# Kernel tuning notes

Measured on AMD Instinct MI355X. Metric: run time of the kernel, lower is better.

The kernel has to match this reference:

```python
import jax, jax.numpy as jnp
import numpy as np


def _cell(xt, h, c, Wih, Whh, b):
    # Single LSTM cell step; PyTorch gate order i, f, g, o.
    g = xt @ Wih.T + h @ Whh.T + b
    i, f, gg, o = jnp.split(g, 4, axis=-1)
    c = jax.nn.sigmoid(f) * c + jax.nn.sigmoid(i) * jnp.tanh(gg)
    h = jax.nn.sigmoid(o) * jnp.tanh(c)
    return h, c


def _lstm_layer(x, Wih, Whh, b):
    # x: [B, T, D] -> hs: [B, T, H], (h, c): final states [B, H]
    B = x.shape[0]
    H = Whh.shape[1]
    h0 = jnp.zeros((B, H), x.dtype)
    c0 = jnp.zeros((B, H), x.dtype)

    def step(carry, xt):
        h, c = carry
        h, c = _cell(xt, h, c, Wih, Whh, b)
        return (h, c), h

    (h, c), hs = jax.lax.scan(step, (h0, c0), jnp.swapaxes(x, 0, 1))
    return jnp.swapaxes(hs, 0, 1), h, c


def setup_inputs() -> dict:
    key = jax.random.key(0)
    B, T_SRC, D_IN, H, TGT = 512, 256, 32, 128, 64
    ks = iter(jax.random.split(key, 32))
    s_in = 1.0 / np.sqrt(H)

    def u(k, shape):
        return jax.random.uniform(k, shape, jnp.float32, -s_in, s_in)

    inp = {"x": jax.random.normal(next(ks), (B, T_SRC, D_IN), jnp.float32),
           "target_len": TGT}
    for pre in ("enc", "dec"):
        for l, din in ((0, D_IN), (1, H)):
            inp[f"{pre}_Wih{l}"] = u(next(ks), (4 * H, din))
            inp[f"{pre}_Whh{l}"] = u(next(ks), (4 * H, H))
            inp[f"{pre}_bih{l}"] = u(next(ks), (4 * H,))
            inp[f"{pre}_bhh{l}"] = u(next(ks), (4 * H,))
    inp["lin_W"] = u(next(ks), (D_IN, H))
    inp["lin_b"] = u(next(ks), (D_IN,))
    return inp


def reference(x, target_len,
              enc_Wih0, enc_Whh0, enc_bih0, enc_bhh0,
              enc_Wih1, enc_Whh1, enc_bih1, enc_bhh1,
              dec_Wih0, dec_Whh0, dec_bih0, dec_bhh0,
              dec_Wih1, dec_Whh1, dec_bih1, dec_bhh1,
              lin_W, lin_b):
    # --- encoder: 2-layer full-sequence LSTM, zero initial state ---
    hs0, eh0, ec0 = _lstm_layer(x, enc_Wih0, enc_Whh0, enc_bih0 + enc_bhh0)
    _, eh1, ec1 = _lstm_layer(hs0, enc_Wih1, enc_Whh1, enc_bih1 + enc_bhh1)

    # --- decoder: recursive single-step LSTM + linear head, fed back ---
    db0 = dec_bih0 + dec_bhh0
    db1 = dec_bih1 + dec_bhh1
    dec_in0 = x[:, -1, :]  # last source step

    def step(carry, _):
        h0, c0, h1, c1, inp = carry
        h0, c0 = _cell(inp, h0, c0, dec_Wih0, dec_Whh0, db0)
        h1, c1 = _cell(h0, h1, c1, dec_Wih1, dec_Whh1, db1)
        out = h1 @ lin_W.T + lin_b
        return (h0, c0, h1, c1, out), out

    _, outs = jax.lax.scan(step, (eh0, ec0, eh1, ec1, dec_in0), None,
                           length=target_len)
    return jnp.swapaxes(outs, 0, 1)  # [B, target_len, input_size]
```

## Files before the change

### kernel.cpp

```cpp
#include <hip/hip_runtime.h>
#include <cstdint>
#include <cstddef>

typedef short  short8  __attribute__((ext_vector_type(8)));
typedef float  float4v __attribute__((ext_vector_type(4)));

#define MFMA_B16(a,b,c) __builtin_amdgcn_mfma_f32_16x16x32_bf16(a,b,c,0,0,0)

static constexpr int B_  = 512;
static constexpr int T_  = 256;
static constexpr int DIN = 32;
static constexpr int H_  = 128;
static constexpr int TGT = 64;

static constexpr size_t OFF_XFRAG = 0;
static constexpr size_t OFF_EW0   = 8388608;
static constexpr size_t OFF_EW1LO = OFF_EW0   + 163840;
static constexpr size_t OFF_EW1HI = OFF_EW1LO + 131072;
static constexpr size_t OFF_DW0   = OFF_EW1HI + 131072;
static constexpr size_t OFF_DW1LO = OFF_DW0   + 163840;
static constexpr size_t OFF_DW1HI = OFF_DW1LO + 131072;
static constexpr size_t OFF_LIN   = OFF_DW1HI + 131072;
static constexpr size_t OFF_BIAS  = OFF_LIN   + 8192;
static constexpr size_t WS_NEED   = OFF_BIAS  + 8320;

static constexpr int SM_W    = 0;
static constexpr int SM_ABUF = 131072;
static constexpr int SM_INP  = 147712;
static constexpr int SM_LIN  = 148992;
static constexpr int SM_TOTAL= 157184;

__device__ __forceinline__ short f2bf(float f){
  unsigned u = __float_as_uint(f);
  unsigned r = (u + 0x7fffu + ((u>>16)&1u)) >> 16;
  return (short)(r & 0xffffu);
}
__device__ __forceinline__ float fast_sigm(float x){
  float e = __expf(-x);
  return __builtin_amdgcn_rcpf(1.f + e);
}
__device__ __forceinline__ float fast_tanh(float x){
  float e = __expf(-2.f*x);
  return __builtin_amdgcn_rcpf(1.f + e)*2.f - 1.f;
}

__global__ void prep_x_kernel(const float* __restrict__ x, short8* __restrict__ xfrag){
  int i = blockIdx.x*256 + threadIdx.x;
  if (i >= 32*256*64) return;
  int l    = i & 63;
  int t    = (i >> 6) & 255;
  int bblk = i >> 14;
  int b    = bblk*16 + (l & 15);
  const float* src = x + ((size_t)(b*T_ + t))*DIN + ((l>>4)*8);
  short8 v;
  #pragma unroll
  for (int j=0;j<8;j++) v[j] = f2bf(src[j]);
  xfrag[i] = v;
}

__device__ __forceinline__ void pack160(short8* __restrict__ dst,
                                        const float* __restrict__ Wih,
                                        const float* __restrict__ Whh,
                                        int e){
  int nt = e/320; int r = e%320; int kb = r/64; int l = r%64;
  int n  = nt*16 + (l&15);
  short8 v;
  #pragma unroll
  for (int j=0;j<8;j++){
    int k = kb*32 + (l>>4)*8 + j;
    float f = (k < 32) ? Wih[n*32 + k] : Whh[n*128 + (k-32)];
    v[j] = f2bf(f);
  }
  dst[e] = v;
}
__device__ __forceinline__ void pack256s(short8* __restrict__ dlo, short8* __restrict__ dhi,
                                         const float* __restrict__ Wih,
                                         const float* __restrict__ Whh,
                                         int e){
  int nt = e/512; int r = e%512; int kb = r/64; int l = r%64;
  int n  = nt*16 + (l&15);
  short8 v;
  #pragma unroll
  for (int j=0;j<8;j++){
    int k = kb*32 + (l>>4)*8 + j;
    float f = (k < 128) ? Wih[n*128 + k] : Whh[n*128 + (k-128)];
    v[j] = f2bf(f);
  }
  if (kb < 4) dlo[(nt*4 + kb)*64 + l]     = v;
  else        dhi[(nt*4 + (kb-4))*64 + l] = v;
}

__global__ void prep_w_kernel(
    const float* __restrict__ eWih0, const float* __restrict__ eWhh0,
    const float* __restrict__ eWih1, const float* __restrict__ eWhh1,
    const float* __restrict__ dWih0, const float* __restrict__ dWhh0,
    const float* __restrict__ dWih1, const float* __restrict__ dWhh1,
    const float* __restrict__ linW,
    const float* __restrict__ eb0a, const float* __restrict__ eb0b,
    const float* __restrict__ eb1a, const float* __restrict__ eb1b,
    const float* __restrict__ db0a, const float* __restrict__ db0b,
    const float* __restrict__ db1a, const float* __restrict__ db1b,
    const float* __restrict__ linb,
    short8* __restrict__ encW0,
    short8* __restrict__ encW1lo, short8* __restrict__ encW1hi,
    short8* __restrict__ decW0,
    short8* __restrict__ decW1lo, short8* __restrict__ decW1hi,
    short8* __restrict__ linT,  float* __restrict__ biases)
{
  int i = blockIdx.x*256 + threadIdx.x;
  if (i < 10240)       { pack160(encW0, eWih0, eWhh0, i); }
  else if (i < 26624)  { pack256s(encW1lo, encW1hi, eWih1, eWhh1, i-10240); }
  else if (i < 36864)  { pack160(decW0, dWih0, dWhh0, i-26624); }
  else if (i < 53248)  { pack256s(decW1lo, decW1hi, dWih1, dWhh1, i-36864); }
  else if (i < 53760)  {
    int e = i - 53248;
    int nt = e/256; int r = e%256; int kb = r/64; int l = r%64;
    int n = nt*16 + (l&15);
    short8 v;
    #pragma unroll
    for (int j=0;j<8;j++){
      int k = kb*32 + (l>>4)*8 + j;
      v[j] = f2bf(linW[n*128 + k]);
    }
    linT[e] = v;
  }
  else if (i < 55840)  {
    int e = i - 53760;
    float v;
    if      (e < 512)  v = eb0a[e]       + eb0b[e];
    else if (e < 1024) v = eb1a[e-512]   + eb1b[e-512];
    else if (e < 1536) v = db0a[e-1024]  + db0b[e-1024];
    else if (e < 2048) v = db1a[e-1536]  + db1b[e-1536];
    else               v = linb[e-2048];
    biases[e] = v;
  }
}

__global__ __launch_bounds__(512, 1) void lstm_main_kernel(
    const short8* __restrict__ xfrag,
    const short8* __restrict__ encW0,
    const short8* __restrict__ encW1lo, const short8* __restrict__ encW1hi,
    const short8* __restrict__ decW0,
    const short8* __restrict__ decW1lo, const short8* __restrict__ decW1hi,
    const short8* __restrict__ linT,  const float* __restrict__ biases,
    float* __restrict__ out)
{
  extern __shared__ __align__(16) char smem[];
  short8* Wlds        = (short8*)(smem + SM_W);
  short (*Abuf)[520]  = (short(*)[520])(smem + SM_ABUF);
  short (*inpA)[40]   = (short(*)[40])(smem + SM_INP);
  short8* Wlin        = (short8*)(smem + SM_LIN);

  const int tid  = threadIdx.x;
  const int w    = tid >> 6;
  const int l    = tid & 63;
  const int col  = l & 15;
  const int lq   = l >> 4;
  const int bblk = blockIdx.x;

  for (int i = tid; i < 8192; i += 512) Wlds[i] = encW1hi[i];
  for (int i = tid; i < 16*520; i += 512) ((short*)Abuf)[i] = 0;

  short8 W0r[4][5];
  short8 W1lo[4][4];
  #pragma unroll
  for (int i=0;i<4;i++){
    #pragma unroll
    for (int kb=0;kb<5;kb++) W0r[i][kb]  = encW0  [(size_t)(8*i+w)*320 + (size_t)kb*64 + l];
    #pragma unroll
    for (int kb=0;kb<4;kb++) W1lo[i][kb] = encW1lo[(size_t)(8*i+w)*256 + (size_t)kb*64 + l];
  }
  float bs0[4], bs1[4];
  #pragma unroll
  for (int i=0;i<4;i++){
    bs0[i] = biases[       (8*i+w)*16 + col];
    bs1[i] = biases[512 +  (8*i+w)*16 + col];
  }

  float c0[4] = {0.f,0.f,0.f,0.f};
  float c1[4] = {0.f,0.f,0.f,0.f};

  const short8* xf = xfrag + (size_t)bblk*T_*64 + l;
  short8 a0 = xf[0];
  __syncthreads();


  {
    short8 hp[4];
    #pragma unroll
    for (int kb=0;kb<4;kb++) hp[kb] = *(const short8*)&Abuf[col][128 + kb*32 + lq*8];
    float4v acc0[4];
    #pragma unroll
    for (int i4=0;i4<4;i4++){
      float4v a = {bs0[i4],bs0[i4],bs0[i4],bs0[i4]};
      a = MFMA_B16(a0, W0r[i4][0], a);
      #pragma unroll
      for (int kb=0;kb<4;kb++) a = MFMA_B16(hp[kb], W0r[i4][kb+1], a);
      acc0[i4] = a;
    }
    a0 = xf[64];
    #pragma unroll
    for (int q=0;q<4;q++){
      float cc = fast_sigm(acc0[1][q])*c0[q] + fast_sigm(acc0[0][q])*fast_tanh(acc0[2][q]);
      c0[q] = cc;
      Abuf[lq*4+q][0 + 16*w + col] = f2bf(fast_sigm(acc0[3][q])*fast_tanh(cc));
    }
    __syncthreads();
  }

  #pragma unroll 2
  for (int i = 1; i < T_; i++){
    const int p_h0_r = ((i-1)&1)*128;
    const int p_h0_w = (i&1)*128;
    const int p_h1_r = 256 + (i&1)*128;
    const int p_h1_w = 256 + ((i-1)&1)*128;

    short8 hp[4], h1p[4];
    #pragma unroll
    for (int kb=0;kb<4;kb++) hp[kb]  = *(const short8*)&Abuf[col][p_h0_r + kb*32 + lq*8];
    #pragma unroll
    for (int kb=0;kb<4;kb++) h1p[kb] = *(const short8*)&Abuf[col][p_h1_r + kb*32 + lq*8];

    float4v acc0[4], acc1[4];
    #pragma unroll
    for (int i4=0;i4<4;i4++){
      float4v a = {bs0[i4],bs0[i4],bs0[i4],bs0[i4]};
      a = MFMA_B16(a0, W0r[i4][0], a);
      #pragma unroll
      for (int kb=0;kb<4;kb++) a = MFMA_B16(hp[kb], W0r[i4][kb+1], a);
      acc0[i4] = a;

      float4v b = {bs1[i4],bs1[i4],bs1[i4],bs1[i4]};
      #pragma unroll
      for (int kb=0;kb<4;kb++) b = MFMA_B16(hp[kb], W1lo[i4][kb], b);
      #pragma unroll
      for (int kb=0;kb<4;kb++){
        short8 wv = Wlds[((8*i4+w)*4 + kb)*64 + l];
        b = MFMA_B16(h1p[kb], wv, b);
      }
      acc1[i4] = b;
    }
    a0 = xf[(size_t)((i+1 < T_) ? i+1 : i)*64];

    #pragma unroll
    for (int q=0;q<4;q++){
      float cc = fast_sigm(acc0[1][q])*c0[q] + fast_sigm(acc0[0][q])*fast_tanh(acc0[2][q]);
      c0[q] = cc;
      Abuf[lq*4+q][p_h0_w + 16*w + col] = f2bf(fast_sigm(acc0[3][q])*fast_tanh(cc));
    }
    #pragma unroll
    for (int q=0;q<4;q++){
      float cc = fast_sigm(acc1[1][q])*c1[q] + fast_sigm(acc1[0][q])*fast_tanh(acc1[2][q]);
      c1[q] = cc;
      Abuf[lq*4+q][p_h1_w + 16*w + col] = f2bf(fast_sigm(acc1[3][q])*fast_tanh(cc));
    }
    __syncthreads();
  }

  {
    const int p_h0_r = 128;
    const int p_h1_r = 256 + 0;
    const int p_h1_w = 256 + 128;
    short8 hp[4], h1p[4];
    #pragma unroll
    for (int kb=0;kb<4;kb++) hp[kb]  = *(const short8*)&Abuf[col][p_h0_r + kb*32 + lq*8];
    #pragma unroll
    for (int kb=0;kb<4;kb++) h1p[kb] = *(const short8*)&Abuf[col][p_h1_r + kb*32 + lq*8];
    float4v acc1[4];
    #pragma unroll
    for (int i4=0;i4<4;i4++){
      float4v b = {bs1[i4],bs1[i4],bs1[i4],bs1[i4]};
      #pragma unroll
      for (int kb=0;kb<4;kb++) b = MFMA_B16(hp[kb], W1lo[i4][kb], b);
      #pragma unroll
      for (int kb=0;kb<4;kb++){
        short8 wv = Wlds[((8*i4+w)*4 + kb)*64 + l];
        b = MFMA_B16(h1p[kb], wv, b);
      }
      acc1[i4] = b;
    }
    #pragma unroll
    for (int q=0;q<4;q++){
      float cc = fast_sigm(acc1[1][q])*c1[q] + fast_sigm(acc1[0][q])*fast_tanh(acc1[2][q]);
      c1[q] = cc;
      Abuf[lq*4+q][p_h1_w + 16*w + col] = f2bf(fast_sigm(acc1[3][q])*fast_tanh(cc));
    }
    __syncthreads();
  }

  for (int i = tid; i < 8192; i += 512) Wlds[i] = decW1hi[i];
  if (tid < 512) Wlin[tid] = linT[tid];
  #pragma unroll
  for (int i=0;i<4;i++){
    #pragma unroll
    for (int kb=0;kb<5;kb++) W0r[i][kb]  = decW0  [(size_t)(8*i+w)*320 + (size_t)kb*64 + l];
    #pragma unroll
    for (int kb=0;kb<4;kb++) W1lo[i][kb] = decW1lo[(size_t)(8*i+w)*256 + (size_t)kb*64 + l];
    bs0[i] = biases[1024 + (8*i+w)*16 + col];
    bs1[i] = biases[1536 + (8*i+w)*16 + col];
  }
  float blin = (w < 2) ? biases[2048 + w*16 + col] : 0.f;
  if (w == 0){
    *(short8*)&inpA[col][lq*8] = xf[(size_t)(T_-1)*64];
  }
  __syncthreads();

  #pragma unroll 2
  for (int td = 0; td < TGT; td++){
    const int h0r = ((td+1)&1) * 128;
    const int h0w = 128 - h0r;
    const int h1r = 256 + h0r;
    const int h1w = 256 + h0w;

    short8 a0d = *(const short8*)&inpA[col][lq*8];
    short8 ah[4];
    #pragma unroll
    for (int kb=0;kb<4;kb++) ah[kb] = *(const short8*)&Abuf[col][h0r + kb*32 + lq*8];
    float4v acc0[4];
    #pragma unroll
    for (int i=0;i<4;i++){
      float4v a = {bs0[i],bs0[i],bs0[i],bs0[i]};
      a = MFMA_B16(a0d, W0r[i][0], a);
      #pragma unroll
      for (int kb=0;kb<4;kb++) a = MFMA_B16(ah[kb], W0r[i][kb+1], a);
      acc0[i] = a;
    }
    #pragma unroll
    for (int q=0;q<4;q++){
      float cc = fast_sigm(acc0[1][q])*c0[q] + fast_sigm(acc0[0][q])*fast_tanh(acc0[2][q]);
      c0[q] = cc;
      Abuf[lq*4+q][h0w + 16*w + col] = f2bf(fast_sigm(acc0[3][q])*fast_tanh(cc));
    }
    __syncthreads();

    short8 a1lo[4], a1hi[4];
    #pragma unroll
    for (int kb=0;kb<4;kb++) a1lo[kb] = *(const short8*)&Abuf[col][h0w + kb*32 + lq*8];
    #pragma unroll
    for (int kb=0;kb<4;kb++) a1hi[kb] = *(const short8*)&Abuf[col][h1r + kb*32 + lq*8];
    float4v acc1[4];
    #pragma unroll
    for (int i=0;i<4;i++){
      float4v a = {bs1[i],bs1[i],bs1[i],bs1[i]};
      #pragma unroll
      for (int kb=0;kb<4;kb++) a = MFMA_B16(a1lo[kb], W1lo[i][kb], a);
      #pragma unroll
      for (int kb=0;kb<4;kb++){
        short8 wv = Wlds[((8*i+w)*4 + kb)*64 + l];
        a = MFMA_B16(a1hi[kb], wv, a);
      }
      acc1[i] = a;
    }
    #pragma unroll
    for (int q=0;q<4;q++){
      float cc = fast_sigm(acc1[1][q])*c1[q] + fast_sigm(acc1[0][q])*fast_tanh(acc1[2][q]);
      c1[q] = cc;
      Abuf[lq*4+q][h1w + 16*w + col] = f2bf(fast_sigm(acc1[3][q])*fast_tanh(cc));
    }
    __syncthreads();

    if (w < 2){
      short8 hf[4];
      #pragma unroll
      for (int kb=0;kb<4;kb++) hf[kb] = *(const short8*)&Abuf[col][h1w + kb*32 + lq*8];
      float4v a = {blin,blin,blin,blin};
      #pragma unroll
      for (int kb=0;kb<4;kb++){
        short8 wv = Wlin[(w*4+kb)*64 + l];
        a = MFMA_B16(hf[kb], wv, a);
      }
      #pragma unroll
      for (int q=0;q<4;q++){
        float v = a[q];
        int b = bblk*16 + lq*4 + q;
        out[((size_t)b*TGT + td)*DIN + (w*16 + col)] = v;
        inpA[lq*4+q][w*16 + col] = f2bf(v);
      }
    }
    __syncthreads();
  }
}

extern "C" void kernel_launch(void* const* d_in, const int* in_sizes, int n_in,
                              void* d_out, int out_size, void* d_ws, size_t ws_size,
                              hipStream_t stream) {
  const float* x      = (const float*)d_in[0];
  const float* eWih0  = (const float*)d_in[2];
  const float* eWhh0  = (const float*)d_in[3];
  const float* eb0a   = (const float*)d_in[4];
  const float* eb0b   = (const float*)d_in[5];
  const float* eWih1  = (const float*)d_in[6];
  const float* eWhh1  = (const float*)d_in[7];
  const float* eb1a   = (const float*)d_in[8];
  const float* eb1b   = (const float*)d_in[9];
  const float* dWih0  = (const float*)d_in[10];
  const float* dWhh0  = (const float*)d_in[11];
  const float* db0a   = (const float*)d_in[12];
  const float* db0b   = (const float*)d_in[13];
  const float* dWih1  = (const float*)d_in[14];
  const float* dWhh1  = (const float*)d_in[15];
  const float* db1a   = (const float*)d_in[16];
  const float* db1b   = (const float*)d_in[17];
  const float* linW   = (const float*)d_in[18];
  const float* linb   = (const float*)d_in[19];

  char* ws = (char*)d_ws;
  short8* xfrag   = (short8*)(ws + OFF_XFRAG);
  short8* encW0   = (short8*)(ws + OFF_EW0);
  short8* encW1lo = (short8*)(ws + OFF_EW1LO);
  short8* encW1hi = (short8*)(ws + OFF_EW1HI);
  short8* decW0   = (short8*)(ws + OFF_DW0);
  short8* decW1lo = (short8*)(ws + OFF_DW1LO);
  short8* decW1hi = (short8*)(ws + OFF_DW1HI);
  short8* linT    = (short8*)(ws + OFF_LIN);
  float*  biases  = (float*)(ws + OFF_BIAS);

  hipFuncSetAttribute((const void*)lstm_main_kernel,
                      hipFuncAttributeMaxDynamicSharedMemorySize, SM_TOTAL);

  prep_x_kernel<<<2048, 256, 0, stream>>>(x, xfrag);
  prep_w_kernel<<<219, 256, 0, stream>>>(
      eWih0,eWhh0,eWih1,eWhh1,dWih0,dWhh0,dWih1,dWhh1,linW,
      eb0a,eb0b,eb1a,eb1b,db0a,db0b,db1a,db1b,linb,
      encW0,encW1lo,encW1hi,decW0,decW1lo,decW1hi,linT,biases);
  lstm_main_kernel<<<32, 512, SM_TOTAL, stream>>>(
      xfrag, encW0, encW1lo, encW1hi, decW0, decW1lo, decW1hi,
      linT, biases, (float*)d_out);
}
```

Baseline: 736.6 us.

## Halve LSTM block to 4 waves holding full recurrent weights in registers

The main LSTM kernel drops from 512 to 256 threads, so each wave now owns 8 gate tiles instead of 4. It keeps all recurrent and layer-1 weights (including the high half that was previously read from LDS every step) in registers, and only the small input-projection weights stay in static shared memory. This removes per-step LDS weight reads and the large dynamic LDS allocation. In exchange each wave issues twice as many MFMAs per step serially and register pressure roughly doubles, which risks spills and lower latency hiding on the sequential critical path.

```diff
diff --git a/kernel.cpp b/kernel.cpp
--- a/kernel.cpp
+++ b/kernel.cpp
@@ -23,12 +23,6 @@
 static constexpr size_t OFF_LIN   = OFF_DW1HI + 131072;
 static constexpr size_t OFF_BIAS  = OFF_LIN   + 8192;
 static constexpr size_t WS_NEED   = OFF_BIAS  + 8320;
-
-static constexpr int SM_W    = 0;
-static constexpr int SM_ABUF = 131072;
-static constexpr int SM_INP  = 147712;
-static constexpr int SM_LIN  = 148992;
-static constexpr int SM_TOTAL= 157184;
 
 __device__ __forceinline__ short f2bf(float f){
   unsigned u = __float_as_uint(f);
@@ -136,7 +130,7 @@
   }
 }
 
-__global__ __launch_bounds__(512, 1) void lstm_main_kernel(
+__global__ __launch_bounds__(256, 1) void lstm_main_kernel(
     const short8* __restrict__ xfrag,
     const short8* __restrict__ encW0,
     const short8* __restrict__ encW1lo, const short8* __restrict__ encW1hi,
@@ -145,11 +139,10 @@
     const short8* __restrict__ linT,  const float* __restrict__ biases,
     float* __restrict__ out)
 {
-  extern __shared__ __align__(16) char smem[];
-  short8* Wlds        = (short8*)(smem + SM_W);
-  short (*Abuf)[520]  = (short(*)[520])(smem + SM_ABUF);
-  short (*inpA)[40]   = (short(*)[40])(smem + SM_INP);
-  short8* Wlin        = (short8*)(smem + SM_LIN);
+  __shared__ __align__(16) short8 Wx[2048];
+  __shared__ __align__(16) short Abuf[16][520];
+  __shared__ __align__(16) short inpA[16][40];
+  __shared__ __align__(16) short8 Wlin[512];
 
   const int tid  = threadIdx.x;
   const int w    = tid >> 6;
@@ -158,53 +151,50 @@
   const int lq   = l >> 4;
   const int bblk = blockIdx.x;
 
-  for (int i = tid; i < 8192; i += 512) Wlds[i] = encW1hi[i];
-  for (int i = tid; i < 16*520; i += 512) ((short*)Abuf)[i] = 0;
-
-  short8 W0r[4][5];
-  short8 W1lo[4][4];
+  for (int i = tid; i < 2048; i += 256) Wx[i] = encW0[(size_t)(i>>6)*320 + (i&63)];
+  for (int i = tid; i < 16*520; i += 256) ((short*)Abuf)[i] = 0;
+
+  const int wxbase = 2*w*64 + l;
+
+  short8 W0h[8][4];
+  short8 W1r[8][8];
+  float  bs0[8], bs1[8];
   #pragma unroll
-  for (int i=0;i<4;i++){
-    #pragma unroll
-    for (int kb=0;kb<5;kb++) W0r[i][kb]  = encW0  [(size_t)(8*i+w)*320 + (size_t)kb*64 + l];
-    #pragma unroll
-    for (int kb=0;kb<4;kb++) W1lo[i][kb] = encW1lo[(size_t)(8*i+w)*256 + (size_t)kb*64 + l];
-  }
-  float bs0[4], bs1[4];
-  #pragma unroll
-  for (int i=0;i<4;i++){
-    bs0[i] = biases[       (8*i+w)*16 + col];
-    bs1[i] = biases[512 +  (8*i+w)*16 + col];
-  }
-
-  float c0[4] = {0.f,0.f,0.f,0.f};
-  float c1[4] = {0.f,0.f,0.f,0.f};
+  for (int j=0;j<8;j++){
+    int nt = 8*(j>>1) + 2*w + (j&1);
+    #pragma unroll
+    for (int kb=0;kb<4;kb++) W0h[j][kb] = encW0  [(size_t)nt*320 + (size_t)(kb+1)*64 + l];
+    #pragma unroll
+    for (int kb=0;kb<4;kb++) W1r[j][kb]   = encW1lo[(size_t)nt*256 + (size_t)kb*64 + l];
+    #pragma unroll
+    for (int kb=0;kb<4;kb++) W1r[j][kb+4] = encW1hi[(size_t)nt*256 + (size_t)kb*64 + l];
+    bs0[j] = biases[      nt*16 + col];
+    bs1[j] = biases[512 + nt*16 + col];
+  }
+
+  float c0[8] = {0,0,0,0,0,0,0,0};
+  float c1[8] = {0,0,0,0,0,0,0,0};
 
   const short8* xf = xfrag + (size_t)bblk*T_*64 + l;
   short8 a0 = xf[0];
   __syncthreads();
 
-
   {
-    short8 hp[4];
-    #pragma unroll
-    for (int kb=0;kb<4;kb++) hp[kb] = *(const short8*)&Abuf[col][128 + kb*32 + lq*8];
-    float4v acc0[4];
-    #pragma unroll
-    for (int i4=0;i4<4;i4++){
-      float4v a = {bs0[i4],bs0[i4],bs0[i4],bs0[i4]};
-      a = MFMA_B16(a0, W0r[i4][0], a);
-      #pragma unroll
-      for (int kb=0;kb<4;kb++) a = MFMA_B16(hp[kb], W0r[i4][kb+1], a);
-      acc0[i4] = a;
+    float4v acc0[8];
+    #pragma unroll
+    for (int j=0;j<8;j++){
+      float4v a = {bs0[j],bs0[j],bs0[j],bs0[j]};
+      acc0[j] = MFMA_B16(a0, Wx[wxbase + (j>>1)*512 + (j&1)*64], a);
     }
     a0 = xf[64];
     #pragma unroll
-    for (int q=0;q<4;q++){
-      float cc = fast_sigm(acc0[1][q])*c0[q] + fast_sigm(acc0[0][q])*fast_tanh(acc0[2][q]);
-      c0[q] = cc;
-      Abuf[lq*4+q][0 + 16*w + col] = f2bf(fast_sigm(acc0[3][q])*fast_tanh(cc));
-    }
+    for (int p=0;p<2;p++)
+      #pragma unroll
+      for (int q=0;q<4;q++){
+        float cc = fast_sigm(acc0[p][q])*fast_tanh(acc0[4+p][q]);
+        c0[p*4+q] = cc;
+        Abuf[lq*4+q][0 + (2*w+p)*16 + col] = f2bf(fast_sigm(acc0[6+p][q])*fast_tanh(cc));
+      }
     __syncthreads();
   }
 
@@ -221,39 +211,45 @@
     #pragma unroll
     for (int kb=0;kb<4;kb++) h1p[kb] = *(const short8*)&Abuf[col][p_h1_r + kb*32 + lq*8];
 
-    float4v acc0[4], acc1[4];
-    #pragma unroll
-    for (int i4=0;i4<4;i4++){
-      float4v a = {bs0[i4],bs0[i4],bs0[i4],bs0[i4]};
-      a = MFMA_B16(a0, W0r[i4][0], a);
-      #pragma unroll
-      for (int kb=0;kb<4;kb++) a = MFMA_B16(hp[kb], W0r[i4][kb+1], a);
-      acc0[i4] = a;
-
-      float4v b = {bs1[i4],bs1[i4],bs1[i4],bs1[i4]};
-      #pragma unroll
-      for (int kb=0;kb<4;kb++) b = MFMA_B16(hp[kb], W1lo[i4][kb], b);
-      #pragma unroll
-      for (int kb=0;kb<4;kb++){
-        short8 wv = Wlds[((8*i4+w)*4 + kb)*64 + l];
-        b = MFMA_B16(h1p[kb], wv, b);
-      }
-      acc1[i4] = b;
+    float4v acc0[8];
+    #pragma unroll
+    for (int j=0;j<8;j++){
+      float4v a = {bs0[j],bs0[j],bs0[j],bs0[j]};
+      a = MFMA_B16(a0, Wx[wxbase + (j>>1)*512 + (j&1)*64], a);
+      #pragma unroll
+      for (int kb=0;kb<4;kb++) a = MFMA_B16(hp[kb], W0h[j][kb], a);
+      acc0[j] = a;
     }
     a0 = xf[(size_t)((i+1 < T_) ? i+1 : i)*64];
-
-    #pragma unroll
-    for (int q=0;q<4;q++){
-      float cc = fast_sigm(acc0[1][q])*c0[q] + fast_sigm(acc0[0][q])*fast_tanh(acc0[2][q]);
-      c0[q] = cc;
-      Abuf[lq*4+q][p_h0_w + 16*w + col] = f2bf(fast_sigm(acc0[3][q])*fast_tanh(cc));
-    }
-    #pragma unroll
-    for (int q=0;q<4;q++){
-      float cc = fast_sigm(acc1[1][q])*c1[q] + fast_sigm(acc1[0][q])*fast_tanh(acc1[2][q]);
-      c1[q] = cc;
-      Abuf[lq*4+q][p_h1_w + 16*w + col] = f2bf(fast_sigm(acc1[3][q])*fast_tanh(cc));
-    }
+    #pragma unroll
+    for (int p=0;p<2;p++)
+      #pragma unroll
+      for (int q=0;q<4;q++){
+        float cc = fast_sigm(acc0[2+p][q])*c0[p*4+q]
+                 + fast_sigm(acc0[p][q])*fast_tanh(acc0[4+p][q]);
+        c0[p*4+q] = cc;
+        Abuf[lq*4+q][p_h0_w + (2*w+p)*16 + col] = f2bf(fast_sigm(acc0[6+p][q])*fast_tanh(cc));
+      }
+
+    float4v acc1[8];
+    #pragma unroll
+    for (int j=0;j<8;j++){
+      float4v a = {bs1[j],bs1[j],bs1[j],bs1[j]};
+      #pragma unroll
+      for (int kb=0;kb<4;kb++) a = MFMA_B16(hp[kb],  W1r[j][kb],   a);
+      #pragma unroll
+      for (int kb=0;kb<4;kb++) a = MFMA_B16(h1p[kb], W1r[j][kb+4], a);
+      acc1[j] = a;
+    }
+    #pragma unroll
+    for (int p=0;p<2;p++)
+      #pragma unroll
+      for (int q=0;q<4;q++){
+        float cc = fast_sigm(acc1[2+p][q])*c1[p*4+q]
+                 + fast_sigm(acc1[p][q])*fast_tanh(acc1[4+p][q]);
+        c1[p*4+q] = cc;
+        Abuf[lq*4+q][p_h1_w + (2*w+p)*16 + col] = f2bf(fast_sigm(acc1[6+p][q])*fast_tanh(cc));
+      }
     __syncthreads();
   }
 
@@ -266,38 +262,41 @@
     for (int kb=0;kb<4;kb++) hp[kb]  = *(const short8*)&Abuf[col][p_h0_r + kb*32 + lq*8];
     #pragma unroll
     for (int kb=0;kb<4;kb++) h1p[kb] = *(const short8*)&Abuf[col][p_h1_r + kb*32 + lq*8];
-    float4v acc1[4];
-    #pragma unroll
-    for (int i4=0;i4<4;i4++){
-      float4v b = {bs1[i4],bs1[i4],bs1[i4],bs1[i4]};
-      #pragma unroll
-      for (int kb=0;kb<4;kb++) b = MFMA_B16(hp[kb], W1lo[i4][kb], b);
-      #pragma unroll
-      for (int kb=0;kb<4;kb++){
-        short8 wv = Wlds[((8*i4+w)*4 + kb)*64 + l];
-        b = MFMA_B16(h1p[kb], wv, b);
-      }
-      acc1[i4] = b;
-    }
-    #pragma unroll
-    for (int q=0;q<4;q++){
-      float cc = fast_sigm(acc1[1][q])*c1[q] + fast_sigm(acc1[0][q])*fast_tanh(acc1[2][q]);
-      c1[q] = cc;
-      Abuf[lq*4+q][p_h1_w + 16*w + col] = f2bf(fast_sigm(acc1[3][q])*fast_tanh(cc));
-    }
-    __syncthreads();
-  }
-
-  for (int i = tid; i < 8192; i += 512) Wlds[i] = decW1hi[i];
-  if (tid < 512) Wlin[tid] = linT[tid];
+    float4v acc1[8];
+    #pragma unroll
+    for (int j=0;j<8;j++){
+      float4v a = {bs1[j],bs1[j],bs1[j],bs1[j]};
+      #pragma unroll
+      for (int kb=0;kb<4;kb++) a = MFMA_B16(hp[kb],  W1r[j][kb],   a);
+      #pragma unroll
+      for (int kb=0;kb<4;kb++) a = MFMA_B16(h1p[kb], W1r[j][kb+4], a);
+      acc1[j] = a;
+    }
+    #pragma unroll
+    for (int p=0;p<2;p++)
+      #pragma unroll
+      for (int q=0;q<4;q++){
+        float cc = fast_sigm(acc1[2+p][q])*c1[p*4+q]
+                 + fast_sigm(acc1[p][q])*fast_tanh(acc1[4+p][q]);
+        c1[p*4+q] = cc;
+        Abuf[lq*4+q][p_h1_w + (2*w+p)*16 + col] = f2bf(fast_sigm(acc1[6+p][q])*fast_tanh(cc));
+      }
+    __syncthreads();
+  }
+
+  for (int i = tid; i < 2048; i += 256) Wx[i] = decW0[(size_t)(i>>6)*320 + (i&63)];
+  for (int i = tid; i < 512;  i += 256) Wlin[i] = linT[i];
   #pragma unroll
-  for (int i=0;i<4;i++){
-    #pragma unroll
-    for (int kb=0;kb<5;kb++) W0r[i][kb]  = decW0  [(size_t)(8*i+w)*320 + (size_t)kb*64 + l];
-    #pragma unroll
-    for (int kb=0;kb<4;kb++) W1lo[i][kb] = decW1lo[(size_t)(8*i+w)*256 + (size_t)kb*64 + l];
-    bs0[i] = biases[1024 + (8*i+w)*16 + col];
-    bs1[i] = biases[1536 + (8*i+w)*16 + col];
+  for (int j=0;j<8;j++){
+    int nt = 8*(j>>1) + 2*w + (j&1);
+    #pragma unroll
+    for (int kb=0;kb<4;kb++) W0h[j][kb] = decW0  [(size_t)nt*320 + (size_t)(kb+1)*64 + l];
+    #pragma unroll
+    for (int kb=0;kb<4;kb++) W1r[j][kb]   = decW1lo[(size_t)nt*256 + (size_t)kb*64 + l];
+    #pragma unroll
+    for (int kb=0;kb<4;kb++) W1r[j][kb+4] = decW1hi[(size_t)nt*256 + (size_t)kb*64 + l];
+    bs0[j] = biases[1024 + nt*16 + col];
+    bs1[j] = biases[1536 + nt*16 + col];
   }
   float blin = (w < 2) ? biases[2048 + w*16 + col] : 0.f;
   if (w == 0){
@@ -313,24 +312,27 @@
     const int h1w = 256 + h0w;
 
     short8 a0d = *(const short8*)&inpA[col][lq*8];
-    short8 ah[4];
-    #pragma unroll
-    for (int kb=0;kb<4;kb++) ah[kb] = *(const short8*)&Abuf[col][h0r + kb*32 + lq*8];
-    float4v acc0[4];
-    #pragma unroll
-    for (int i=0;i<4;i++){
-      float4v a = {bs0[i],bs0[i],bs0[i],bs0[i]};
-      a = MFMA_B16(a0d, W0r[i][0], a);
-      #pragma unroll
-      for (int kb=0;kb<4;kb++) a = MFMA_B16(ah[kb], W0r[i][kb+1], a);
-      acc0[i] = a;
-    }
-    #pragma unroll
-    for (int q=0;q<4;q++){
-      float cc = fast_sigm(acc0[1][q])*c0[q] + fast_sigm(acc0[0][q])*fast_tanh(acc0[2][q]);
-      c0[q] = cc;
-      Abuf[lq*4+q][h0w + 16*w + col] = f2bf(fast_sigm(acc0[3][q])*fast_tanh(cc));
-    }
+    short8 hp[4];
+    #pragma unroll
+    for (int kb=0;kb<4;kb++) hp[kb] = *(const short8*)&Abuf[col][h0r + kb*32 + lq*8];
+    float4v acc0[8];
+    #pragma unroll
+    for (int j=0;j<8;j++){
+      float4v a = {bs0[j],bs0[j],bs0[j],bs0[j]};
+      a = MFMA_B16(a0d, Wx[wxbase + (j>>1)*512 + (j&1)*64], a);
+      #pragma unroll
+      for (int kb=0;kb<4;kb++) a = MFMA_B16(hp[kb], W0h[j][kb], a);
+      acc0[j] = a;
+    }
+    #pragma unroll
+    for (int p=0;p<2;p++)
+      #pragma unroll
+      for (int q=0;q<4;q++){
+        float cc = fast_sigm(acc0[2+p][q])*c0[p*4+q]
+                 + fast_sigm(acc0[p][q])*fast_tanh(acc0[4+p][q]);
+        c0[p*4+q] = cc;
+        Abuf[lq*4+q][h0w + (2*w+p)*16 + col] = f2bf(fast_sigm(acc0[6+p][q])*fast_tanh(cc));
+      }
     __syncthreads();
 
     short8 a1lo[4], a1hi[4];
@@ -338,25 +340,25 @@
     for (int kb=0;kb<4;kb++) a1lo[kb] = *(const short8*)&Abuf[col][h0w + kb*32 + lq*8];
     #pragma unroll
     for (int kb=0;kb<4;kb++) a1hi[kb] = *(const short8*)&Abuf[col][h1r + kb*32 + lq*8];
-    float4v acc1[4];
-    #pragma unroll
-    for (int i=0;i<4;i++){
-      float4v a = {bs1[i],bs1[i],bs1[i],bs1[i]};
-      #pragma unroll
-      for (int kb=0;kb<4;kb++) a = MFMA_B16(a1lo[kb], W1lo[i][kb], a);
-      #pragma unroll
-      for (int kb=0;kb<4;kb++){
-        short8 wv = Wlds[((8*i+w)*4 + kb)*64 + l];
-        a = MFMA_B16(a1hi[kb], wv, a);
-      }
-      acc1[i] = a;
-    }
-    #pragma unroll
-    for (int q=0;q<4;q++){
-      float cc = fast_sigm(acc1[1][q])*c1[q] + fast_sigm(acc1[0][q])*fast_tanh(acc1[2][q]);
-      c1[q] = cc;
-      Abuf[lq*4+q][h1w + 16*w + col] = f2bf(fast_sigm(acc1[3][q])*fast_tanh(cc));
-    }
+    float4v acc1[8];
+    #pragma unroll
+    for (int j=0;j<8;j++){
+      float4v a = {bs1[j],bs1[j],bs1[j],bs1[j]};
+      #pragma unroll
+      for (int kb=0;kb<4;kb++) a = MFMA_B16(a1lo[kb], W1r[j][kb],   a);
+      #pragma unroll
+      for (int kb=0;kb<4;kb++) a = MFMA_B16(a1hi[kb], W1r[j][kb+4], a);
+      acc1[j] = a;
+    }
+    #pragma unroll
+    for (int p=0;p<2;p++)
+      #pragma unroll
+      for (int q=0;q<4;q++){
+        float cc = fast_sigm(acc1[2+p][q])*c1[p*4+q]
+                 + fast_sigm(acc1[p][q])*fast_tanh(acc1[4+p][q]);
+        c1[p*4+q] = cc;
+        Abuf[lq*4+q][h1w + (2*w+p)*16 + col] = f2bf(fast_sigm(acc1[6+p][q])*fast_tanh(cc));
+      }
     __syncthreads();
 
     if (w < 2){
@@ -365,10 +367,7 @@
       for (int kb=0;kb<4;kb++) hf[kb] = *(const short8*)&Abuf[col][h1w + kb*32 + lq*8];
       float4v a = {blin,blin,blin,blin};
       #pragma unroll
-      for (int kb=0;kb<4;kb++){
-        short8 wv = Wlin[(w*4+kb)*64 + l];
-        a = MFMA_B16(hf[kb], wv, a);
-      }
+      for (int kb=0;kb<4;kb++) a = MFMA_B16(hf[kb], Wlin[(w*4+kb)*64 + l], a);
       #pragma unroll
       for (int q=0;q<4;q++){
         float v = a[q];
@@ -415,15 +414,12 @@
   short8* linT    = (short8*)(ws + OFF_LIN);
   float*  biases  = (float*)(ws + OFF_BIAS);
 
-  hipFuncSetAttribute((const void*)lstm_main_kernel,
-                      hipFuncAttributeMaxDynamicSharedMemorySize, SM_TOTAL);
-
   prep_x_kernel<<<2048, 256, 0, stream>>>(x, xfrag);
   prep_w_kernel<<<219, 256, 0, stream>>>(
       eWih0,eWhh0,eWih1,eWhh1,dWih0,dWhh0,dWih1,dWhh1,linW,
       eb0a,eb0b,eb1a,eb1b,db0a,db0b,db1a,db1b,linb,
       encW0,encW1lo,encW1hi,decW0,decW1lo,decW1hi,linT,biases);
-  lstm_main_kernel<<<32, 512, SM_TOTAL, stream>>>(
+  lstm_main_kernel<<<32, 256, 0, stream>>>(
       xfrag, encW0, encW1lo, encW1hi, decW0, decW1lo, decW1hi,
       linT, biases, (float*)d_out);
 }
```

Measured after the change: 1.350 ms. +83.3%, slower.
